# Optimization experiments

Measured on AMD Instinct MI355X. Metric: run time of the kernel, lower is better.

Reference implementation:

```python
import jax, jax.numpy as jnp
from jax import lax
import numpy as np

NODE = 100000
D = 256      # input_dim
H = 256      # hidden_dim
P = 4096     # num paths between the pair
L = 8        # path length (hops)
OUT = 1


def setup_inputs() -> dict:
    key = jax.random.key(0)
    ks = jax.random.split(key, 10)
    s = 1.0 / np.sqrt(H)
    return {
        "embedding": jax.random.normal(ks[0], (NODE, D), jnp.float32) * 0.1,
        "w_ih": jax.random.normal(ks[1], (4 * H, D), jnp.float32) * s,
        "w_hh": jax.random.normal(ks[2], (4 * H, H), jnp.float32) * s,
        "b_ih": jax.random.normal(ks[3], (4 * H,), jnp.float32) * s,
        "b_hh": jax.random.normal(ks[4], (4 * H,), jnp.float32) * s,
        "w_lin": jax.random.normal(ks[5], (OUT, H + 2 * D), jnp.float32) * 0.05,
        "b_lin": jax.random.normal(ks[6], (OUT,), jnp.float32) * 0.05,
        "paths": jax.random.randint(ks[7], (P, L), 0, NODE, jnp.int64),
        "user_id": jax.random.randint(ks[8], (1,), 0, NODE, jnp.int64),
        "item_id": jax.random.randint(ks[9], (1,), 0, NODE, jnp.int64),
    }


def _lstm_final_hidden(x, w_ih, w_hh, b_ih, b_hh):
    # x: [P, L, D] -> final hidden state h_n: [P, H] (PyTorch gate order i,f,g,o)
    p, _, _ = x.shape
    h = x.shape  # noqa (shape comment)
    hidden = w_hh.shape[1]
    b = b_ih + b_hh

    def step(carry, x_t):
        h, c = carry
        gates = x_t @ w_ih.T + h @ w_hh.T + b  # [P, 4H]
        i, f, g, o = jnp.split(gates, 4, axis=-1)
        c = jax.nn.sigmoid(f) * c + jax.nn.sigmoid(i) * jnp.tanh(g)
        h = jax.nn.sigmoid(o) * jnp.tanh(c)
        return (h, c), None

    h0 = jnp.zeros((p, hidden), x.dtype)
    c0 = jnp.zeros((p, hidden), x.dtype)
    (h_n, _), _ = lax.scan(step, (h0, c0), jnp.swapaxes(x, 0, 1))  # scan over L
    return h_n


def reference(embedding, w_ih, w_hh, b_ih, b_hh, w_lin, b_lin, paths, user_id, item_id):
    # Batched version of the per-path loop: embed all paths, one LSTM scan.
    x = embedding[paths]                                   # [P, L, D]
    sum_hidden = _lstm_final_hidden(x, w_ih, w_hh, b_ih, b_hh)  # [P, H] (== stacked h_n)

    # MaxPool2d((1, H)) over hidden dim -> attention logits over paths
    att = jnp.max(sum_hidden, axis=-1, keepdims=True)      # [P, 1]
    att = jax.nn.softmax(att, axis=0)                      # softmax over paths
    path_emb = jnp.sum(sum_hidden * att, axis=0, keepdims=True)  # [1, H]

    user_emb = embedding[user_id]                          # [1, D]
    item_emb = embedding[item_id]                          # [1, D]
    emb = jnp.concatenate([user_emb, item_emb, path_emb], axis=-1)  # [1, 2D+H]
    out = jax.nn.sigmoid(emb @ w_lin.T + b_lin)            # [1, OUT]
    return out
```

## Files before the change

### kernel.cpp

```cpp
#include <hip/hip_runtime.h>
#include <stdint.h>

#define NPATHS 4096
#define LPATH  8
#define DIM    256
#define HID    256
#define KDIM   512
#define NGATE  1024

typedef short  short4v __attribute__((ext_vector_type(4)));
typedef short  short8v __attribute__((ext_vector_type(8)));
typedef float  float4v __attribute__((ext_vector_type(4)));

__device__ __forceinline__ unsigned short f2bf(float f) {
    union { float f; uint32_t u; } v; v.f = f;
    uint32_t u = v.u;
    u += 0x7FFFu + ((u >> 16) & 1u);
    return (unsigned short)(u >> 16);
}

__device__ __forceinline__ float fast_sigmoid(float x) {
    return 1.0f / (1.0f + __expf(-x));
}
__device__ __forceinline__ float fast_tanh(float x) {
    x = fminf(15.0f, fmaxf(-15.0f, x));
    float e = __expf(2.0f * x);
    return (e - 1.0f) / (e + 1.0f);
}

__device__ __forceinline__ unsigned int encf(float f) {
    unsigned int u = __float_as_uint(f);
    return (u & 0x80000000u) ? ~u : (u | 0x80000000u);
}

__device__ __forceinline__ void dma16(void* lds, const void* g) {
    typedef const unsigned int __attribute__((address_space(1)))* gp_t;
    typedef unsigned int __attribute__((address_space(3)))* lp_t;
    gp_t gp = reinterpret_cast<gp_t>(reinterpret_cast<uintptr_t>(g));
    lp_t lp = reinterpret_cast<lp_t>(static_cast<unsigned int>(reinterpret_cast<uintptr_t>(lds)));
    __builtin_amdgcn_global_load_lds(gp, lp, 16, 0, 0);
}

__global__ void prep_kernel(const float* __restrict__ w_ih, const float* __restrict__ w_hh,
                            const float* __restrict__ b_ih, const float* __restrict__ b_hh,
                            unsigned short* __restrict__ Wc, float* __restrict__ bias,
                            unsigned int* __restrict__ logits_enc) {
    int gid  = blockIdx.x * blockDim.x + threadIdx.x;
    int base = gid * 4;
    int row  = base >> 9;
    int col  = base & 511;
    const float* src = (col < DIM) ? (w_ih + row * DIM + col)
                                   : (w_hh + row * DIM + (col - DIM));
    float4 v = *(const float4*)src;
    short4v pk = {(short)f2bf(v.x), (short)f2bf(v.y), (short)f2bf(v.z), (short)f2bf(v.w)};
    *(short4v*)(Wc + base) = pk;
    if (gid < NGATE) bias[gid] = b_ih[gid] + b_hh[gid];
    if (gid < NPATHS) logits_enc[gid] = 0u;
}

__global__ void gather_kernel(const float* __restrict__ embedding,
                              const int* __restrict__ paths,
                              unsigned short* __restrict__ Xb) {
    int gid = blockIdx.x * 256 + threadIdx.x;
    int row = gid >> 6;
    int seg = gid & 63;
    int p = row & (NPATHS - 1);
    int t = row >> 12;
    int node = paths[p * LPATH + t];
    float4 v = *(const float4*)(embedding + (size_t)node * DIM + seg * 4);
    short4v pk = {(short)f2bf(v.x), (short)f2bf(v.y), (short)f2bf(v.z), (short)f2bf(v.w)};
    *(short4v*)(Xb + (size_t)row * DIM + seg * 4) = pk;
}

template<bool FIRST, bool LAST>
__global__ __launch_bounds__(256, 1)
void step_kernel(const unsigned short* __restrict__ Xb,
                 const unsigned short* __restrict__ Wc,
                 const float* __restrict__ bias,
                 const unsigned short* __restrict__ h_in,
                 unsigned short* __restrict__ h_outp,
                 float* __restrict__ c_g,
                 float* __restrict__ h_fin,
                 unsigned int* __restrict__ logits_enc,
                 int t) {
    __shared__ short sA[2][128 * 32];
    __shared__ short sB[2][128 * 32];
    __shared__ short hT[128 * 40];

    const int tid  = threadIdx.x;
    const int wave = tid >> 6;
    const int lane = tid & 63;
    const int l15  = lane & 15;
    const int quad = lane >> 4;
    const int pt = blockIdx.x >> 3;
    const int ut = blockIdx.x & 7;
    const int p0 = pt * 128;

    const int NITER = FIRST ? 8 : 16;

    const char* XbB = (const char*)Xb + (size_t)t * NPATHS * DIM * 2;
    const char* hB  = (const char*)h_in;
    const char* WcB = (const char*)Wc;

    const int fl0 = tid * 16, fl1 = 4096 + tid * 16;
    const int rA0 = fl0 >> 6, cb0 = fl0 & 63;
    const int rA1 = fl1 >> 6, cb1 = fl1 & 63;
    const int wr0 = ((rA0 >> 5) << 8) + ut * 32 + (rA0 & 31);
    const int wr1 = ((rA1 >> 5) << 8) + ut * 32 + (rA1 & 31);

    float4v acc[2][8];
    const float4v zero4 = {0.0f, 0.0f, 0.0f, 0.0f};
#pragma unroll
    for (int i = 0; i < 2; ++i)
#pragma unroll
        for (int j = 0; j < 8; ++j) acc[i][j] = zero4;

    auto issue = [&](int kc) {
        int buf = kc & 1;
        const char* abase = (kc < 8) ? XbB : hB;
        int ko = (kc & 7) * 64;
        dma16(&sA[buf][fl0 >> 1], abase + (size_t)(p0 + rA0) * 512 + ko + cb0);
        dma16(&sA[buf][fl1 >> 1], abase + (size_t)(p0 + rA1) * 512 + ko + cb1);
        dma16(&sB[buf][fl0 >> 1], WcB + (size_t)wr0 * 1024 + kc * 64 + cb0);
        dma16(&sB[buf][fl1 >> 1], WcB + (size_t)wr1 * 1024 + kc * 64 + cb1);
    };

    issue(0);
    for (int kc = 0; kc < NITER; ++kc) {
        __syncthreads();
        if (kc + 1 < NITER) issue(kc + 1);
        int buf = kc & 1;
        const short* Ab = &sA[buf][(wave * 32 + l15) * 32 + quad * 8];
        short8v a0 = *(const short8v*)(Ab);
        short8v a1 = *(const short8v*)(Ab + 16 * 32);
#pragma unroll
        for (int ct = 0; ct < 8; ++ct) {
            short8v b = *(const short8v*)(&sB[buf][(ct * 16 + l15) * 32 + quad * 8]);
            acc[0][ct] = __builtin_amdgcn_mfma_f32_16x16x32_bf16(a0, b, acc[0][ct], 0, 0, 0);
            acc[1][ct] = __builtin_amdgcn_mfma_f32_16x16x32_bf16(a1, b, acc[1][ct], 0, 0, 0);
        }
    }

    float pmax[8];
#pragma unroll
    for (int j = 0; j < 8; ++j) pmax[j] = -1e30f;

#pragma unroll
    for (int rt = 0; rt < 2; ++rt) {
#pragma unroll
        for (int uh = 0; uh < 2; ++uh) {
            int u  = ut * 32 + uh * 16 + l15;
            float bi = bias[0 * HID + u];
            float bfv = bias[1 * HID + u];
            float bg = bias[2 * HID + u];
            float bo = bias[3 * HID + u];
            int prow = wave * 32 + rt * 16 + quad * 4;
            float* cptr = c_g + (size_t)u * NPATHS + p0 + prow;
            float4 cold;
            if (!FIRST) cold = *(const float4*)cptr;
            float4 cnew, hv;
#pragma unroll
            for (int r = 0; r < 4; ++r) {
                float iv = acc[rt][0 * 2 + uh][r] + bi;
                float fv = acc[rt][1 * 2 + uh][r] + bfv;
                float gv = acc[rt][2 * 2 + uh][r] + bg;
                float ov = acc[rt][3 * 2 + uh][r] + bo;
                float cp = FIRST ? 0.0f : (&cold.x)[r];
                float cn = fast_sigmoid(fv) * cp + fast_sigmoid(iv) * fast_tanh(gv);
                (&cnew.x)[r] = cn;
                float h = fast_sigmoid(ov) * fast_tanh(cn);
                (&hv.x)[r] = h;
                pmax[rt * 4 + r] = fmaxf(pmax[rt * 4 + r], h);
            }
            *(float4*)cptr = cnew;
            if (!LAST) {
#pragma unroll
                for (int r = 0; r < 4; ++r)
                    hT[(prow + r) * 40 + uh * 16 + l15] = (short)f2bf((&hv.x)[r]);
            } else {
                *(float4*)(h_fin + (size_t)u * NPATHS + p0 + prow) = hv;
            }
        }
    }

    if (!LAST) {
        __syncthreads();
#pragma unroll
        for (int i = 0; i < 2; ++i) {
            int cid = i * 256 + tid;
            int row = cid >> 2, seg = cid & 3;
            short8v v = *(const short8v*)(&hT[row * 40 + seg * 8]);
            *(short8v*)(h_outp + (size_t)(p0 + row) * HID + ut * 32 + seg * 8) = v;
        }
    } else {
#pragma unroll
        for (int j = 0; j < 8; ++j) {
            float m = pmax[j];
            m = fmaxf(m, __shfl_xor(m, 1, 64));
            m = fmaxf(m, __shfl_xor(m, 2, 64));
            m = fmaxf(m, __shfl_xor(m, 4, 64));
            m = fmaxf(m, __shfl_xor(m, 8, 64));
            if (l15 == 0) {
                int rt = j >> 2, r = j & 3;
                int p = p0 + wave * 32 + rt * 16 + quad * 4 + r;
                atomicMax(&logits_enc[p], encf(m));
            }
        }
    }
}

__global__ void softmax_kernel(const unsigned int* __restrict__ enc,
                               float* __restrict__ pw) {
    __shared__ float red[256];
    int tid = threadIdx.x;
    float vals[16];
    float m = -1e30f;
#pragma unroll
    for (int i = 0; i < 16; ++i) {
        unsigned int u = enc[i * 256 + tid];
        float f = (u & 0x80000000u) ? __uint_as_float(u ^ 0x80000000u)
                                    : __uint_as_float(~u);
        vals[i] = f;
        m = fmaxf(m, f);
    }
    red[tid] = m; __syncthreads();
    for (int s = 128; s > 0; s >>= 1) {
        if (tid < s) red[tid] = fmaxf(red[tid], red[tid + s]);
        __syncthreads();
    }
    m = red[0]; __syncthreads();
    float e[16];
    float sum = 0.0f;
#pragma unroll
    for (int i = 0; i < 16; ++i) { e[i] = __expf(vals[i] - m); sum += e[i]; }
    red[tid] = sum; __syncthreads();
    for (int s = 128; s > 0; s >>= 1) {
        if (tid < s) red[tid] += red[tid + s];
        __syncthreads();
    }
    float invZ = 1.0f / red[0];
#pragma unroll
    for (int i = 0; i < 16; ++i) pw[i * 256 + tid] = e[i] * invZ;
}

__global__ void attn_kernel(const float* __restrict__ h_fin,
                            const float* __restrict__ pw,
                            float* __restrict__ path_emb) {
    __shared__ float red[256];
    int u = blockIdx.x, tid = threadIdx.x;
    const float* row = h_fin + (size_t)u * NPATHS;
    float acc = 0.0f;
    for (int p = tid; p < NPATHS; p += 256) acc += pw[p] * row[p];
    red[tid] = acc; __syncthreads();
    for (int s = 128; s > 0; s >>= 1) {
        if (tid < s) red[tid] += red[tid + s];
        __syncthreads();
    }
    if (tid == 0) path_emb[u] = red[0];
}

__global__ void final_kernel(const float* __restrict__ embedding,
                             const int* __restrict__ user_id,
                             const int* __restrict__ item_id,
                             const float* __restrict__ w_lin,
                             const float* __restrict__ b_lin,
                             const float* __restrict__ path_emb,
                             float* __restrict__ out) {
    __shared__ float red[256];
    int tid = threadIdx.x;
    int u  = user_id[0];
    int it = item_id[0];
    float s = w_lin[tid]       * embedding[(size_t)u  * DIM + tid]
            + w_lin[256 + tid] * embedding[(size_t)it * DIM + tid]
            + w_lin[512 + tid] * path_emb[tid];
    red[tid] = s; __syncthreads();
    for (int st = 128; st > 0; st >>= 1) {
        if (tid < st) red[tid] += red[tid + st];
        __syncthreads();
    }
    if (tid == 0) out[0] = 1.0f / (1.0f + __expf(-(red[0] + b_lin[0])));
}

extern "C" void kernel_launch(void* const* d_in, const int* in_sizes, int n_in,
                              void* d_out, int out_size, void* d_ws, size_t ws_size,
                              hipStream_t stream) {
    const float* embedding = (const float*)d_in[0];
    const float* w_ih      = (const float*)d_in[1];
    const float* w_hh      = (const float*)d_in[2];
    const float* b_ih      = (const float*)d_in[3];
    const float* b_hh      = (const float*)d_in[4];
    const float* w_lin     = (const float*)d_in[5];
    const float* b_lin     = (const float*)d_in[6];
    const int*   paths     = (const int*)d_in[7];
    const int*   user_id   = (const int*)d_in[8];
    const int*   item_id   = (const int*)d_in[9];
    float* outp = (float*)d_out;

    char* ws = (char*)d_ws;
    size_t off = 0;
    auto alloc = [&](size_t n) { void* p = ws + off; off = (off + n + 255) & ~(size_t)255; return p; };
    unsigned short* Wc        = (unsigned short*)alloc(NGATE * KDIM * 2);
    float*          bias      = (float*)alloc(NGATE * 4);
    unsigned int*   logits_enc= (unsigned int*)alloc(NPATHS * 4);
    float*          pw        = (float*)alloc(NPATHS * 4);
    float*          path_emb  = (float*)alloc(HID * 4);
    unsigned short* Xb        = (unsigned short*)alloc((size_t)LPATH * NPATHS * DIM * 2);
    unsigned short* h_buf     = (unsigned short*)alloc((size_t)2 * NPATHS * HID * 2);
    float*          c_g       = (float*)alloc((size_t)HID * NPATHS * 4);
    float*          h_fin     = (float*)alloc((size_t)HID * NPATHS * 4);

    prep_kernel<<<512, 256, 0, stream>>>(w_ih, w_hh, b_ih, b_hh, Wc, bias, logits_enc);
    gather_kernel<<<8192, 256, 0, stream>>>(embedding, paths, Xb);

    for (int t = 0; t < LPATH; ++t) {
        const unsigned short* hin = h_buf + (size_t)(t & 1) * NPATHS * HID;
        unsigned short*      hout = h_buf + (size_t)((t + 1) & 1) * NPATHS * HID;
        if (t == 0)
            step_kernel<true, false><<<256, 256, 0, stream>>>(Xb, Wc, bias, hin, hout,
                                                              c_g, h_fin, logits_enc, t);
        else if (t == LPATH - 1)
            step_kernel<false, true><<<256, 256, 0, stream>>>(Xb, Wc, bias, hin, hout,
                                                              c_g, h_fin, logits_enc, t);
        else
            step_kernel<false, false><<<256, 256, 0, stream>>>(Xb, Wc, bias, hin, hout,
                                                               c_g, h_fin, logits_enc, t);
    }

    softmax_kernel<<<1, 256, 0, stream>>>(logits_enc, pw);
    attn_kernel<<<HID, 256, 0, stream>>>(h_fin, pw, path_emb);
    final_kernel<<<1, 256, 0, stream>>>(embedding, user_id, item_id, w_lin, b_lin,
                                        path_emb, outp);
}
```

Before: 283.7 us.

## Restructure LSTM step kernel with register-resident weights and fused prep/gather

The step kernel now uses 64x64 path-by-unit tiles. Each wave keeps its gate weight fragments in registers, pre-packed in an MFMA-friendly layout, and the whole A tile is loaded into LDS once instead of double-buffered per K chunk. The prep and gather kernels are merged into one launch. The attention stage now reads the final bf16 hidden state directly and accumulates with atomics, which removes the fp32 h_fin buffer and the per-path weight array. This cuts launches and global traffic, but the kernel needs far more registers, and the final hidden state now feeds attention in bf16, which lowers precision.

```diff
diff --git a/kernel.cpp b/kernel.cpp
--- a/kernel.cpp
+++ b/kernel.cpp
@@ -5,8 +5,6 @@
 #define LPATH  8
 #define DIM    256
 #define HID    256
-#define KDIM   512
-#define NGATE  1024
 
 typedef short  short4v __attribute__((ext_vector_type(4)));
 typedef short  short8v __attribute__((ext_vector_type(8)));
@@ -18,7 +16,9 @@
     u += 0x7FFFu + ((u >> 16) & 1u);
     return (unsigned short)(u >> 16);
 }
-
+__device__ __forceinline__ float bf2f(unsigned short s) {
+    return __uint_as_float(((uint32_t)s) << 16);
+}
 __device__ __forceinline__ float fast_sigmoid(float x) {
     return 1.0f / (1.0f + __expf(-x));
 }
@@ -27,10 +27,12 @@
     float e = __expf(2.0f * x);
     return (e - 1.0f) / (e + 1.0f);
 }
-
 __device__ __forceinline__ unsigned int encf(float f) {
     unsigned int u = __float_as_uint(f);
     return (u & 0x80000000u) ? ~u : (u | 0x80000000u);
+}
+__device__ __forceinline__ float decf(unsigned int u) {
+    return (u & 0x80000000u) ? __uint_as_float(u & 0x7FFFFFFFu) : __uint_as_float(~u);
 }
 
 __device__ __forceinline__ void dma16(void* lds, const void* g) {
@@ -41,187 +43,167 @@
     __builtin_amdgcn_global_load_lds(gp, lp, 16, 0, 0);
 }
 
-__global__ void prep_kernel(const float* __restrict__ w_ih, const float* __restrict__ w_hh,
+__global__ void prep_gather(const float* __restrict__ w_ih, const float* __restrict__ w_hh,
                             const float* __restrict__ b_ih, const float* __restrict__ b_hh,
-                            unsigned short* __restrict__ Wc, float* __restrict__ bias,
-                            unsigned int* __restrict__ logits_enc) {
-    int gid  = blockIdx.x * blockDim.x + threadIdx.x;
-    int base = gid * 4;
-    int row  = base >> 9;
-    int col  = base & 511;
-    const float* src = (col < DIM) ? (w_ih + row * DIM + col)
-                                   : (w_hh + row * DIM + (col - DIM));
-    float4 v = *(const float4*)src;
-    short4v pk = {(short)f2bf(v.x), (short)f2bf(v.y), (short)f2bf(v.z), (short)f2bf(v.w)};
-    *(short4v*)(Wc + base) = pk;
-    if (gid < NGATE) bias[gid] = b_ih[gid] + b_hh[gid];
-    if (gid < NPATHS) logits_enc[gid] = 0u;
-}
-
-__global__ void gather_kernel(const float* __restrict__ embedding,
-                              const int* __restrict__ paths,
-                              unsigned short* __restrict__ Xb) {
-    int gid = blockIdx.x * 256 + threadIdx.x;
-    int row = gid >> 6;
-    int seg = gid & 63;
-    int p = row & (NPATHS - 1);
-    int t = row >> 12;
-    int node = paths[p * LPATH + t];
-    float4 v = *(const float4*)(embedding + (size_t)node * DIM + seg * 4);
-    short4v pk = {(short)f2bf(v.x), (short)f2bf(v.y), (short)f2bf(v.z), (short)f2bf(v.w)};
-    *(short4v*)(Xb + (size_t)row * DIM + seg * 4) = pk;
+                            const float* __restrict__ embedding, const int* __restrict__ paths,
+                            unsigned short* __restrict__ WfB, float* __restrict__ bias,
+                            unsigned int* __restrict__ logits_enc, float* __restrict__ path_emb,
+                            unsigned short* __restrict__ Xb) {
+    int bid = blockIdx.x;
+    if (bid < 512) {
+        int gid  = bid * 256 + threadIdx.x;
+        int base = gid * 4;
+        int j0   = base & 31;
+        int unit = (base >> 5) & 255;
+        int gkc  = base >> 13;
+        int g    = gkc >> 4, kc = gkc & 15;
+        int row  = g * 256 + unit;
+        int k    = kc * 32 + j0;
+        const float* src = (k < DIM) ? (w_ih + (size_t)row * DIM + k)
+                                     : (w_hh + (size_t)row * HID + (k - DIM));
+        float4 v = *(const float4*)src;
+        short4v pk = {(short)f2bf(v.x), (short)f2bf(v.y), (short)f2bf(v.z), (short)f2bf(v.w)};
+        *(short4v*)(WfB + base) = pk;
+        if (gid < 1024) bias[gid] = b_ih[gid] + b_hh[gid];
+        if (gid < NPATHS) logits_enc[gid] = 0u;
+        if (gid < 256) path_emb[gid] = 0.0f;
+    } else {
+        int gid  = (bid - 512) * 256 + threadIdx.x;
+        int rowt = gid >> 6;
+        int seg  = gid & 63;
+        int p    = rowt & (NPATHS - 1);
+        int t    = rowt >> 12;
+        int node = paths[p * LPATH + t];
+        float4 v = *(const float4*)(embedding + (size_t)node * DIM + seg * 4);
+        short4v pk = {(short)f2bf(v.x), (short)f2bf(v.y), (short)f2bf(v.z), (short)f2bf(v.w)};
+        *(short4v*)(Xb + (size_t)rowt * DIM + seg * 4) = pk;
+    }
 }
 
 template<bool FIRST, bool LAST>
 __global__ __launch_bounds__(256, 1)
 void step_kernel(const unsigned short* __restrict__ Xb,
-                 const unsigned short* __restrict__ Wc,
+                 const unsigned short* __restrict__ WfB,
                  const float* __restrict__ bias,
                  const unsigned short* __restrict__ h_in,
-                 unsigned short* __restrict__ h_outp,
+                 unsigned short* __restrict__ h_out,
                  float* __restrict__ c_g,
-                 float* __restrict__ h_fin,
                  unsigned int* __restrict__ logits_enc,
                  int t) {
-    __shared__ short sA[2][128 * 32];
-    __shared__ short sB[2][128 * 32];
-    __shared__ short hT[128 * 40];
-
-    const int tid  = threadIdx.x;
-    const int wave = tid >> 6;
-    const int lane = tid & 63;
-    const int l15  = lane & 15;
-    const int quad = lane >> 4;
-    const int pt = blockIdx.x >> 3;
-    const int ut = blockIdx.x & 7;
-    const int p0 = pt * 128;
-
-    const int NITER = FIRST ? 8 : 16;
-
-    const char* XbB = (const char*)Xb + (size_t)t * NPATHS * DIM * 2;
-    const char* hB  = (const char*)h_in;
-    const char* WcB = (const char*)Wc;
-
-    const int fl0 = tid * 16, fl1 = 4096 + tid * 16;
-    const int rA0 = fl0 >> 6, cb0 = fl0 & 63;
-    const int rA1 = fl1 >> 6, cb1 = fl1 & 63;
-    const int wr0 = ((rA0 >> 5) << 8) + ut * 32 + (rA0 & 31);
-    const int wr1 = ((rA1 >> 5) << 8) + ut * 32 + (rA1 & 31);
-
-    float4v acc[2][8];
-    const float4v zero4 = {0.0f, 0.0f, 0.0f, 0.0f};
-#pragma unroll
-    for (int i = 0; i < 2; ++i)
-#pragma unroll
-        for (int j = 0; j < 8; ++j) acc[i][j] = zero4;
-
-    auto issue = [&](int kc) {
-        int buf = kc & 1;
-        const char* abase = (kc < 8) ? XbB : hB;
-        int ko = (kc & 7) * 64;
-        dma16(&sA[buf][fl0 >> 1], abase + (size_t)(p0 + rA0) * 512 + ko + cb0);
-        dma16(&sA[buf][fl1 >> 1], abase + (size_t)(p0 + rA1) * 512 + ko + cb1);
-        dma16(&sB[buf][fl0 >> 1], WcB + (size_t)wr0 * 1024 + kc * 64 + cb0);
-        dma16(&sB[buf][fl1 >> 1], WcB + (size_t)wr1 * 1024 + kc * 64 + cb1);
+    __shared__ __align__(16) short sA[64 * 512];
+
+    const int tid   = threadIdx.x;
+    const int wave  = tid >> 6;
+    const int lane  = tid & 63;
+    const int l15   = lane & 15;
+    const int quad  = lane >> 4;
+    const int blk   = blockIdx.x;
+    const int ptile = blk & 63;
+    const int utile = blk >> 6;
+    const int p0    = ptile * 64;
+    const int u0    = utile * 64;
+
+    {
+        const char* xpl = (const char*)Xb + ((size_t)t * NPATHS + p0) * 512;
+        const char* hpl = (const char*)h_in + (size_t)p0 * 512;
+        const char* xl  = xpl + l15 * 512 + quad * 16;
+        const char* hl  = hpl + l15 * 512 + quad * 16;
+#pragma unroll
+        for (int m = 0; m < 16; ++m) {
+            int rf = m >> 2, kq = m & 3;
+            if (FIRST && kq >= 2) continue;
+            int fp = rf * 16 + kq * 4 + wave;
+            const char* base = (kq < 2) ? xl : hl;
+            int kk = ((kq & 1) * 4 + wave) * 64;
+            dma16(sA + fp * 512, base + rf * 8192 + kk);
+        }
+    }
+
+    short8v Bf[4][16];
+    float bb[4];
+    const int unit = u0 + wave * 16 + l15;
+#pragma unroll
+    for (int g = 0; g < 4; ++g) {
+        bb[g] = bias[g * 256 + unit];
+#pragma unroll
+        for (int kc = 0; kc < 16; ++kc)
+            Bf[g][kc] = *(const short8v*)(WfB + (((g * 16 + kc) * 256 + unit) * 32 + quad * 8));
+    }
+
+    __syncthreads();
+
+    float4v acc[4][4];
+    const float4v z4 = {0.0f, 0.0f, 0.0f, 0.0f};
+#pragma unroll
+    for (int rf = 0; rf < 4; ++rf)
+#pragma unroll
+        for (int g = 0; g < 4; ++g) acc[rf][g] = z4;
+
+    auto kstep = [&](int kc) {
+#pragma unroll
+        for (int rf = 0; rf < 4; ++rf) {
+            short8v a = *(const short8v*)(sA + ((rf * 16 + kc) << 9) + lane * 8);
+#pragma unroll
+            for (int g = 0; g < 4; ++g)
+                acc[rf][g] = __builtin_amdgcn_mfma_f32_16x16x32_bf16(
+                    a, Bf[g][kc], acc[rf][g], 0, 0, 0);
+        }
     };
-
-    issue(0);
-    for (int kc = 0; kc < NITER; ++kc) {
-        __syncthreads();
-        if (kc + 1 < NITER) issue(kc + 1);
-        int buf = kc & 1;
-        const short* Ab = &sA[buf][(wave * 32 + l15) * 32 + quad * 8];
-        short8v a0 = *(const short8v*)(Ab);
-        short8v a1 = *(const short8v*)(Ab + 16 * 32);
-#pragma unroll
-        for (int ct = 0; ct < 8; ++ct) {
-            short8v b = *(const short8v*)(&sB[buf][(ct * 16 + l15) * 32 + quad * 8]);
-            acc[0][ct] = __builtin_amdgcn_mfma_f32_16x16x32_bf16(a0, b, acc[0][ct], 0, 0, 0);
-            acc[1][ct] = __builtin_amdgcn_mfma_f32_16x16x32_bf16(a1, b, acc[1][ct], 0, 0, 0);
+    if (FIRST) {
+#pragma unroll
+        for (int kc = 0; kc < 8; ++kc) kstep(kc);
+    } else {
+#pragma unroll
+        for (int kc = 0; kc < 16; ++kc) kstep(kc);
+    }
+
+    float hmax[16];
+#pragma unroll
+    for (int rf = 0; rf < 4; ++rf) {
+#pragma unroll
+        for (int r = 0; r < 4; ++r) {
+            int row = rf * 16 + quad * 4 + r;
+            int idx = rf * 4 + r;
+            float iv = acc[rf][0][r] + bb[0];
+            float fv = acc[rf][1][r] + bb[1];
+            float gv = acc[rf][2][r] + bb[2];
+            float ov = acc[rf][3][r] + bb[3];
+            size_t coff = (size_t)(p0 + row) * HID + unit;
+            float cp = FIRST ? 0.0f : c_g[coff];
+            float cn = fast_sigmoid(fv) * cp + fast_sigmoid(iv) * fast_tanh(gv);
+            if (!LAST) c_g[coff] = cn;
+            float h = fast_sigmoid(ov) * fast_tanh(cn);
+            hmax[idx] = h;
+            h_out[(size_t)(p0 + row) * HID + unit] = f2bf(h);
         }
     }
 
-    float pmax[8];
-#pragma unroll
-    for (int j = 0; j < 8; ++j) pmax[j] = -1e30f;
-
-#pragma unroll
-    for (int rt = 0; rt < 2; ++rt) {
-#pragma unroll
-        for (int uh = 0; uh < 2; ++uh) {
-            int u  = ut * 32 + uh * 16 + l15;
-            float bi = bias[0 * HID + u];
-            float bfv = bias[1 * HID + u];
-            float bg = bias[2 * HID + u];
-            float bo = bias[3 * HID + u];
-            int prow = wave * 32 + rt * 16 + quad * 4;
-            float* cptr = c_g + (size_t)u * NPATHS + p0 + prow;
-            float4 cold;
-            if (!FIRST) cold = *(const float4*)cptr;
-            float4 cnew, hv;
-#pragma unroll
-            for (int r = 0; r < 4; ++r) {
-                float iv = acc[rt][0 * 2 + uh][r] + bi;
-                float fv = acc[rt][1 * 2 + uh][r] + bfv;
-                float gv = acc[rt][2 * 2 + uh][r] + bg;
-                float ov = acc[rt][3 * 2 + uh][r] + bo;
-                float cp = FIRST ? 0.0f : (&cold.x)[r];
-                float cn = fast_sigmoid(fv) * cp + fast_sigmoid(iv) * fast_tanh(gv);
-                (&cnew.x)[r] = cn;
-                float h = fast_sigmoid(ov) * fast_tanh(cn);
-                (&hv.x)[r] = h;
-                pmax[rt * 4 + r] = fmaxf(pmax[rt * 4 + r], h);
-            }
-            *(float4*)cptr = cnew;
-            if (!LAST) {
-#pragma unroll
-                for (int r = 0; r < 4; ++r)
-                    hT[(prow + r) * 40 + uh * 16 + l15] = (short)f2bf((&hv.x)[r]);
-            } else {
-                *(float4*)(h_fin + (size_t)u * NPATHS + p0 + prow) = hv;
-            }
-        }
-    }
-
-    if (!LAST) {
-        __syncthreads();
-#pragma unroll
-        for (int i = 0; i < 2; ++i) {
-            int cid = i * 256 + tid;
-            int row = cid >> 2, seg = cid & 3;
-            short8v v = *(const short8v*)(&hT[row * 40 + seg * 8]);
-            *(short8v*)(h_outp + (size_t)(p0 + row) * HID + ut * 32 + seg * 8) = v;
-        }
-    } else {
-#pragma unroll
-        for (int j = 0; j < 8; ++j) {
-            float m = pmax[j];
+    if (LAST) {
+#pragma unroll
+        for (int idx = 0; idx < 16; ++idx) {
+            float m = hmax[idx];
             m = fmaxf(m, __shfl_xor(m, 1, 64));
             m = fmaxf(m, __shfl_xor(m, 2, 64));
             m = fmaxf(m, __shfl_xor(m, 4, 64));
             m = fmaxf(m, __shfl_xor(m, 8, 64));
             if (l15 == 0) {
-                int rt = j >> 2, r = j & 3;
-                int p = p0 + wave * 32 + rt * 16 + quad * 4 + r;
-                atomicMax(&logits_enc[p], encf(m));
+                int rf = idx >> 2, r = idx & 3;
+                atomicMax(&logits_enc[p0 + rf * 16 + quad * 4 + r], encf(m));
             }
         }
     }
 }
 
-__global__ void softmax_kernel(const unsigned int* __restrict__ enc,
-                               float* __restrict__ pw) {
+__global__ void softmax_prep_kernel(const unsigned int* __restrict__ enc,
+                                    float* __restrict__ scal) {
     __shared__ float red[256];
     int tid = threadIdx.x;
     float vals[16];
     float m = -1e30f;
 #pragma unroll
     for (int i = 0; i < 16; ++i) {
-        unsigned int u = enc[i * 256 + tid];
-        float f = (u & 0x80000000u) ? __uint_as_float(u ^ 0x80000000u)
-                                    : __uint_as_float(~u);
-        vals[i] = f;
-        m = fmaxf(m, f);
+        vals[i] = decf(enc[i * 256 + tid]);
+        m = fmaxf(m, vals[i]);
     }
     red[tid] = m; __syncthreads();
     for (int s = 128; s > 0; s >>= 1) {
@@ -229,34 +211,30 @@
         __syncthreads();
     }
     m = red[0]; __syncthreads();
-    float e[16];
     float sum = 0.0f;
 #pragma unroll
-    for (int i = 0; i < 16; ++i) { e[i] = __expf(vals[i] - m); sum += e[i]; }
+    for (int i = 0; i < 16; ++i) sum += __expf(vals[i] - m);
     red[tid] = sum; __syncthreads();
     for (int s = 128; s > 0; s >>= 1) {
         if (tid < s) red[tid] += red[tid + s];
         __syncthreads();
     }
-    float invZ = 1.0f / red[0];
-#pragma unroll
-    for (int i = 0; i < 16; ++i) pw[i * 256 + tid] = e[i] * invZ;
-}
-
-__global__ void attn_kernel(const float* __restrict__ h_fin,
-                            const float* __restrict__ pw,
-                            float* __restrict__ path_emb) {
-    __shared__ float red[256];
-    int u = blockIdx.x, tid = threadIdx.x;
-    const float* row = h_fin + (size_t)u * NPATHS;
+    if (tid == 0) { scal[0] = m; scal[1] = 1.0f / red[0]; }
+}
+
+__global__ void attn_sum_kernel(const unsigned short* __restrict__ h_final,
+                                const unsigned int* __restrict__ enc,
+                                const float* __restrict__ scal,
+                                float* __restrict__ path_emb) {
+    int tid = threadIdx.x;
+    int p0  = blockIdx.x * 16;
+    float bmax = scal[0], invZ = scal[1];
     float acc = 0.0f;
-    for (int p = tid; p < NPATHS; p += 256) acc += pw[p] * row[p];
-    red[tid] = acc; __syncthreads();
-    for (int s = 128; s > 0; s >>= 1) {
-        if (tid < s) red[tid] += red[tid + s];
-        __syncthreads();
-    }
-    if (tid == 0) path_emb[u] = red[0];
+    for (int p = p0; p < p0 + 16; ++p) {
+        float w = __expf(decf(enc[p]) - bmax) * invZ;
+        acc += w * bf2f(h_final[(size_t)p * HID + tid]);
+    }
+    atomicAdd(&path_emb[tid], acc);
 }
 
 __global__ void final_kernel(const float* __restrict__ embedding,
@@ -299,35 +277,34 @@
     char* ws = (char*)d_ws;
     size_t off = 0;
     auto alloc = [&](size_t n) { void* p = ws + off; off = (off + n + 255) & ~(size_t)255; return p; };
-    unsigned short* Wc        = (unsigned short*)alloc(NGATE * KDIM * 2);
-    float*          bias      = (float*)alloc(NGATE * 4);
+    unsigned short* WfB       = (unsigned short*)alloc((size_t)1024 * 512 * 2);
+    float*          bias      = (float*)alloc(1024 * 4);
     unsigned int*   logits_enc= (unsigned int*)alloc(NPATHS * 4);
-    float*          pw        = (float*)alloc(NPATHS * 4);
+    float*          scal      = (float*)alloc(256);
     float*          path_emb  = (float*)alloc(HID * 4);
     unsigned short* Xb        = (unsigned short*)alloc((size_t)LPATH * NPATHS * DIM * 2);
     unsigned short* h_buf     = (unsigned short*)alloc((size_t)2 * NPATHS * HID * 2);
-    float*          c_g       = (float*)alloc((size_t)HID * NPATHS * 4);
-    float*          h_fin     = (float*)alloc((size_t)HID * NPATHS * 4);
-
-    prep_kernel<<<512, 256, 0, stream>>>(w_ih, w_hh, b_ih, b_hh, Wc, bias, logits_enc);
-    gather_kernel<<<8192, 256, 0, stream>>>(embedding, paths, Xb);
+    float*          c_g       = (float*)alloc((size_t)NPATHS * HID * 4);
+
+    prep_gather<<<8704, 256, 0, stream>>>(w_ih, w_hh, b_ih, b_hh, embedding, paths,
+                                          WfB, bias, logits_enc, path_emb, Xb);
 
     for (int t = 0; t < LPATH; ++t) {
         const unsigned short* hin = h_buf + (size_t)(t & 1) * NPATHS * HID;
         unsigned short*      hout = h_buf + (size_t)((t + 1) & 1) * NPATHS * HID;
         if (t == 0)
-            step_kernel<true, false><<<256, 256, 0, stream>>>(Xb, Wc, bias, hin, hout,
-                                                              c_g, h_fin, logits_enc, t);
+            step_kernel<true, false><<<256, 256, 0, stream>>>(Xb, WfB, bias, hin, hout,
+                                                              c_g, logits_enc, t);
         else if (t == LPATH - 1)
-            step_kernel<false, true><<<256, 256, 0, stream>>>(Xb, Wc, bias, hin, hout,
-                                                              c_g, h_fin, logits_enc, t);
+            step_kernel<false, true><<<256, 256, 0, stream>>>(Xb, WfB, bias, hin, hout,
+                                                              c_g, logits_enc, t);
         else
-            step_kernel<false, false><<<256, 256, 0, stream>>>(Xb, Wc, bias, hin, hout,
-                                                               c_g, h_fin, logits_enc, t);
-    }
-
-    softmax_kernel<<<1, 256, 0, stream>>>(logits_enc, pw);
-    attn_kernel<<<HID, 256, 0, stream>>>(h_fin, pw, path_emb);
+            step_kernel<false, false><<<256, 256, 0, stream>>>(Xb, WfB, bias, hin, hout,
+                                                               c_g, logits_enc, t);
+    }
+
+    softmax_prep_kernel<<<1, 256, 0, stream>>>(logits_enc, scal);
+    attn_sum_kernel<<<NPATHS / 16, 256, 0, stream>>>(h_buf, logits_enc, scal, path_emb);
     final_kernel<<<1, 256, 0, stream>>>(embedding, user_id, item_id, w_lin, b_lin,
                                         path_emb, outp);
 }
```

New measurement: 276.4 us. -2.6%, faster.
